# Optimization experiments

Hardware: AMD Instinct MI355X
Metric: run time of the kernel (lower is better)

## Reference

```python
import jax, jax.numpy as jnp
import numpy as np

B, T, F, U = 64, 256, 256, 1024  # batch, time, input feat, GRU units per layer


def setup_inputs() -> dict:
    key = jax.random.key(0)
    ks = jax.random.split(key, 16)
    rn = lambda k, shape, s: jax.random.normal(k, shape, dtype=jnp.float32) * s
    inp = {"inputs": rn(ks[0], (B, T, F), 1.0)}
    in_dims = [F, U, U]
    for i in range(3):
        inp[f"state{i}"] = rn(ks[1 + i], (B, U), 0.1)
        inp[f"W{i}"] = rn(ks[4 + 3 * i], (in_dims[i], 3 * U), 0.05)  # input kernel [in, 3u]
        inp[f"U{i}"] = rn(ks[5 + 3 * i], (U, 3 * U), 0.05)           # recurrent kernel [u, 3u]
        inp[f"b{i}"] = jnp.zeros((2, 3 * U), dtype=jnp.float32)       # [input_bias; recurrent_bias]
    return inp


def _gru_layer(x, h0, W, Ur, b):
    # Keras GRU, reset_after=True, recurrent_activation=sigmoid, activation=tanh.
    u = h0.shape[-1]
    gx = jnp.einsum('btf,fg->btg', x, W) + b[0]  # precompute input projections for all steps

    def step(h, gxt):
        rec = h @ Ur + b[1]                       # [B, 3u]
        z = jax.nn.sigmoid(gxt[:, :u] + rec[:, :u])
        r = jax.nn.sigmoid(gxt[:, u:2 * u] + rec[:, u:2 * u])
        hh = jnp.tanh(gxt[:, 2 * u:] + r * rec[:, 2 * u:])
        hn = z * h + (1.0 - z) * hh
        return hn, hn

    h_last, ys = jax.lax.scan(step, h0, jnp.swapaxes(gx, 0, 1))  # scan over time
    return jnp.swapaxes(ys, 0, 1), h_last


def reference(inputs, state0, state1, state2, W0, U0, b0, W1, U1, b1, W2, U2, b2):
    x, s0 = _gru_layer(inputs, state0, W0, U0, b0)
    x, s1 = _gru_layer(x, state1, W1, U1, b1)
    x, s2 = _gru_layer(x, state2, W2, U2, b2)
    return x, s0, s1, s2
```

## Files before the change

kernel.cpp:

```cpp
#include <hip/hip_runtime.h>
#include <hip/hip_fp16.h>


typedef _Float16 half8 __attribute__((ext_vector_type(8)));
typedef float f32x4 __attribute__((ext_vector_type(4)));

#define TSTEPS 256
#define UDIM 1024
#define G3U 3072
#define GRIDB 64

__device__ __forceinline__ f32x4 mfma16(half8 a, half8 b, f32x4 c) {
    return __builtin_amdgcn_mfma_f32_16x16x32_f16(a, b, c, 0, 0, 0);
}

__device__ __forceinline__ half8 load_h_agent(const _Float16* p) {
    union { unsigned long long u[2]; half8 h; } un;
    const unsigned long long* q = (const unsigned long long*)p;
    un.u[0] = __hip_atomic_load(q,     __ATOMIC_RELAXED, __HIP_MEMORY_SCOPE_AGENT);
    un.u[1] = __hip_atomic_load(q + 1, __ATOMIC_RELAXED, __HIP_MEMORY_SCOPE_AGENT);
    return un.h;
}

__global__ void f32_to_f16(const float* __restrict__ src, _Float16* __restrict__ dst, int n) {
    int i = blockIdx.x * blockDim.x + threadIdx.x;
    int st = gridDim.x * blockDim.x;
    for (; i < n; i += st) dst[i] = (_Float16)src[i];
}

__global__ void pack_weights(const float* __restrict__ W, const float* __restrict__ Ur,
                             _Float16* __restrict__ Bp, int KIN, int KC) {
    int idx = blockIdx.x * blockDim.x + threadIdx.x;
    int total = 192 * KC * 64;
    int st = gridDim.x * blockDim.x;
    for (; idx < total; idx += st) {
        int lane = idx & 63;
        int kc = (idx >> 6) % KC;
        int nt = idx / (KC * 64);
        int col = nt * 16 + (lane & 15);
        int k0 = kc * 32 + (lane >> 4) * 8;
        half8 v;
#pragma unroll
        for (int i = 0; i < 8; ++i) {
            int k = k0 + i;
            float f = (k < KIN) ? W[(size_t)k * G3U + col]
                                : Ur[(size_t)(k - KIN) * G3U + col];
            v[i] = (_Float16)f;
        }
        *(half8*)(Bp + (size_t)idx * 8) = v;
    }
}

struct LayerArgs {
    const _Float16* xcur;
    const _Float16* h0h;
    const float* state;
    const _Float16* Bp;
    const float* bias;
    _Float16* yown;
    float* fxout;
    float* sout;
    unsigned* own_cnt;
    const unsigned* prod_cnt;
};

using RedT = f32x4 (*)[4][2][64];

template <int KIN, bool XA>
__device__ __forceinline__ void gru_body(const LayerArgs& A, int blk, RedT red) {
    const int tid = threadIdx.x;
    const int lane = tid & 63;
    const int wid = tid >> 6;
    const int col = lane & 15;
    const int lrow = lane >> 4;
    const int klane0 = lrow * 8;
    const int j = blk * 16 + col;
    constexpr int KC = (KIN + UDIM) >> 5;
    constexpr int KCW = KC >> 3;
    constexpr int KINC = KIN >> 5;
    const int ck0 = wid * KCW, ck1 = ck0 + KCW;

    const float b0z = A.bias[j],           b1z = A.bias[G3U + j];
    const float b0r = A.bias[UDIM + j],    b1r = A.bias[G3U + UDIM + j];
    const float b0h = A.bias[2*UDIM + j],  b1h = A.bias[G3U + 2*UDIM + j];

    float hreg[4] = {0.f, 0.f, 0.f, 0.f};
    if (wid < 4) {
#pragma unroll
        for (int e = 0; e < 4; ++e) {
            int m = wid * 16 + lrow * 4 + e;
            hreg[e] = A.state[(size_t)m * UDIM + j];
        }
    }

    const _Float16* bpz = A.Bp + (size_t)(blk)       * KC * 512 + lane * 8;
    const _Float16* bpr = A.Bp + (size_t)(64 + blk)  * KC * 512 + lane * 8;
    const _Float16* bph = A.Bp + (size_t)(128 + blk) * KC * 512 + lane * 8;

    for (int t = 0; t < TSTEPS; ++t) {
        if (tid == 0) {
            if (t > 0) {
                unsigned tgt = (unsigned)(GRIDB * t);
                while (__hip_atomic_load(A.own_cnt, __ATOMIC_RELAXED,
                                         __HIP_MEMORY_SCOPE_AGENT) < tgt)
                    __builtin_amdgcn_s_sleep(2);
            }
            if (XA) {
                unsigned tgt2 = (unsigned)(GRIDB * (t + 1));
                while (__hip_atomic_load(A.prod_cnt, __ATOMIC_RELAXED,
                                         __HIP_MEMORY_SCOPE_AGENT) < tgt2)
                    __builtin_amdgcn_s_sleep(2);
            }
        }
        __syncthreads();

        f32x4 accz[4], accr[4], acchx[4], acchr[4];
#pragma unroll
        for (int m4 = 0; m4 < 4; ++m4) {
            accz[m4] = (f32x4){0.f,0.f,0.f,0.f};
            accr[m4] = (f32x4){0.f,0.f,0.f,0.f};
            acchx[m4] = (f32x4){0.f,0.f,0.f,0.f};
            acchr[m4] = (f32x4){0.f,0.f,0.f,0.f};
        }
        const _Float16* xr[4];
        const _Float16* hr[4];
#pragma unroll
        for (int m4 = 0; m4 < 4; ++m4) {
            int rm = m4 * 16 + (lane & 15);
            xr[m4] = A.xcur + ((size_t)rm * TSTEPS + t) * KIN + klane0;
            hr[m4] = (t == 0) ? (A.h0h + (size_t)rm * UDIM + klane0)
                              : (A.yown + ((size_t)rm * TSTEPS + (t - 1)) * UDIM + klane0);
        }
        int cxe = ck1 < KINC ? ck1 : KINC;
#pragma unroll 2
        for (int ck = ck0; ck < cxe; ++ck) {
            half8 bz = *(const half8*)(bpz + (size_t)ck * 512);
            half8 br = *(const half8*)(bpr + (size_t)ck * 512);
            half8 bh = *(const half8*)(bph + (size_t)ck * 512);
            int off = ck * 32;
#pragma unroll
            for (int m4 = 0; m4 < 4; ++m4) {
                half8 a = XA ? load_h_agent(xr[m4] + off)
                             : *(const half8*)(xr[m4] + off);
                accz[m4]  = mfma16(a, bz, accz[m4]);
                accr[m4]  = mfma16(a, br, accr[m4]);
                acchx[m4] = mfma16(a, bh, acchx[m4]);
            }
        }
        int chs = ck0 > KINC ? ck0 : KINC;
#pragma unroll 2
        for (int ck = chs; ck < ck1; ++ck) {
            half8 bz = *(const half8*)(bpz + (size_t)ck * 512);
            half8 br = *(const half8*)(bpr + (size_t)ck * 512);
            half8 bh = *(const half8*)(bph + (size_t)ck * 512);
            int off = (ck - KINC) * 32;
#pragma unroll
            for (int m4 = 0; m4 < 4; ++m4) {
                half8 a = load_h_agent(hr[m4] + off);
                accz[m4]  = mfma16(a, bz, accz[m4]);
                accr[m4]  = mfma16(a, br, accr[m4]);
                acchr[m4] = mfma16(a, bh, acchr[m4]);
            }
        }

        f32x4 fz = {0.f,0.f,0.f,0.f}, fr = {0.f,0.f,0.f,0.f};
        f32x4 fhx = {0.f,0.f,0.f,0.f}, fhr = {0.f,0.f,0.f,0.f};
        for (int p = 0; p < 2; ++p) {
#pragma unroll
            for (int m4 = 0; m4 < 4; ++m4) {
                red[wid][m4][0][lane] = p ? acchx[m4] : accz[m4];
                red[wid][m4][1][lane] = p ? acchr[m4] : accr[m4];
            }
            __syncthreads();
            if (wid < 4) {
                f32x4 s0 = {0.f,0.f,0.f,0.f}, s1 = {0.f,0.f,0.f,0.f};
#pragma unroll
                for (int s = 0; s < 8; ++s) {
                    s0 += red[s][wid][0][lane];
                    s1 += red[s][wid][1][lane];
                }
                if (p == 0) { fz = s0; fr = s1; } else { fhx = s0; fhr = s1; }
            }
            __syncthreads();
        }

        if (wid < 4) {
#pragma unroll
            for (int e = 0; e < 4; ++e) {
                float zp = fz[e] + b0z + b1z;
                float rp = fr[e] + b0r + b1r;
                float z = 1.f / (1.f + expf(-zp));
                float r = 1.f / (1.f + expf(-rp));
                float hh = tanhf(fhx[e] + b0h + r * (fhr[e] + b1h));
                float hn = z * hreg[e] + (1.f - z) * hh;
                hreg[e] = hn;
                int m = wid * 16 + lrow * 4 + e;
                size_t yi = ((size_t)m * TSTEPS + t) * UDIM + j;
                union { _Float16 f; unsigned short u; } cv;
                cv.f = (_Float16)hn;
                unsigned pu = (unsigned)(unsigned short)__shfl_xor((int)(unsigned)cv.u, 1, 64);
                if (!(col & 1)) {
                    unsigned val = ((unsigned)cv.u) | (pu << 16);
                    __hip_atomic_store((unsigned*)(A.yown + yi), val,
                                       __ATOMIC_RELAXED, __HIP_MEMORY_SCOPE_AGENT);
                }
                if (A.fxout) A.fxout[yi] = hn;
                if (t == TSTEPS - 1) A.sout[(size_t)m * UDIM + j] = hn;
            }
        }

        __syncthreads();
        if (tid == 0)
            __hip_atomic_fetch_add(A.own_cnt, 1u, __ATOMIC_RELAXED,
                                   __HIP_MEMORY_SCOPE_AGENT);
    }
}

__global__ __launch_bounds__(512, 1) void gru_fused(LayerArgs a0, LayerArgs a1, LayerArgs a2) {
    __shared__ f32x4 red[8][4][2][64];
    int lay = blockIdx.x >> 6;
    int blk = blockIdx.x & 63;
    if (lay == 0)      gru_body<256,  false>(a0, blk, red);
    else if (lay == 1) gru_body<1024, true >(a1, blk, red);
    else               gru_body<1024, true >(a2, blk, red);
}

extern "C" void kernel_launch(void* const* d_in, const int* in_sizes, int n_in,
                              void* d_out, int out_size, void* d_ws, size_t ws_size,
                              hipStream_t stream) {
    (void)in_sizes; (void)n_in; (void)out_size; (void)ws_size;

    char* ws = (char*)d_ws;
    size_t off = 0;
    auto take = [&](size_t bytes) -> char* {
        char* p = ws + off;
        off += (bytes + 255) & ~(size_t)255;
        return p;
    };
    unsigned* counters = (unsigned*)take(1024);
    _Float16* h0h0 = (_Float16*)take((size_t)65536 * 2);
    _Float16* h0h1 = (_Float16*)take((size_t)65536 * 2);
    _Float16* h0h2 = (_Float16*)take((size_t)65536 * 2);
    _Float16* xin  = (_Float16*)take((size_t)4194304 * 2);
    _Float16* y0   = (_Float16*)take((size_t)16777216 * 2);
    _Float16* y1   = (_Float16*)take((size_t)16777216 * 2);
    _Float16* y2   = (_Float16*)take((size_t)16777216 * 2);
    _Float16* Bp0  = (_Float16*)take((size_t)192 * 40 * 512 * 2);
    _Float16* Bp1  = (_Float16*)take((size_t)192 * 64 * 512 * 2);
    _Float16* Bp2  = (_Float16*)take((size_t)192 * 64 * 512 * 2);

    hipMemsetAsync(counters, 0, 1024, stream);

    f32_to_f16<<<2048, 256, 0, stream>>>((const float*)d_in[0], xin, 4194304);
    f32_to_f16<<<64, 256, 0, stream>>>((const float*)d_in[1], h0h0, 65536);
    f32_to_f16<<<64, 256, 0, stream>>>((const float*)d_in[5], h0h1, 65536);
    f32_to_f16<<<64, 256, 0, stream>>>((const float*)d_in[9], h0h2, 65536);

    pack_weights<<<1920, 256, 0, stream>>>((const float*)d_in[2], (const float*)d_in[3],
                                           Bp0, 256, 40);
    pack_weights<<<3072, 256, 0, stream>>>((const float*)d_in[6], (const float*)d_in[7],
                                           Bp1, 1024, 64);
    pack_weights<<<3072, 256, 0, stream>>>((const float*)d_in[10], (const float*)d_in[11],
                                           Bp2, 1024, 64);

    float* xout = (float*)d_out;
    float* souts = xout + (size_t)16777216;

    LayerArgs a0 = { xin, h0h0, (const float*)d_in[1], Bp0, (const float*)d_in[4],
                     y0, nullptr, souts + 0, counters + 0, nullptr };
    LayerArgs a1 = { y0, h0h1, (const float*)d_in[5], Bp1, (const float*)d_in[8],
                     y1, nullptr, souts + 65536, counters + 64, counters + 0 };
    LayerArgs a2 = { y1, h0h2, (const float*)d_in[9], Bp2, (const float*)d_in[12],
                     y2, xout, souts + 131072, counters + 128, counters + 64 };

    gru_fused<<<192, 512, 0, stream>>>(a0, a1, a2);
}
```

Before: 5.272 ms.

## Replace global counters with per-block flags and per-wave polling, single reduction pass

Each block now publishes its progress in its own padded flag slot instead of incrementing one shared atomic counter. Every wavefront polls all 64 producer flags itself, and only right before it needs the data. Input-half waves can therefore start on the previous layer's output while hidden-half waves wait on the recurrent state. The two-pass LDS reduction becomes one pass with a single barrier, and the activations use fast __expf formulas. This removes contended atomics and serialized waits from the per-step critical path, at the cost of more polling traffic and slightly reduced precision in the activations.

```diff
diff --git a/kernel.cpp b/kernel.cpp
--- a/kernel.cpp
+++ b/kernel.cpp
@@ -20,6 +20,16 @@
     un.u[0] = __hip_atomic_load(q,     __ATOMIC_RELAXED, __HIP_MEMORY_SCOPE_AGENT);
     un.u[1] = __hip_atomic_load(q + 1, __ATOMIC_RELAXED, __HIP_MEMORY_SCOPE_AGENT);
     return un.h;
+}
+
+__device__ __forceinline__ void poll_flags(const unsigned* f, unsigned tgt) {
+    const unsigned* p = f + (threadIdx.x & 63) * 32;
+    for (;;) {
+        unsigned v = __hip_atomic_load(p, __ATOMIC_RELAXED, __HIP_MEMORY_SCOPE_AGENT);
+        if (__all((int)(v >= tgt))) break;
+        __builtin_amdgcn_s_sleep(2);
+    }
+    asm volatile("" ::: "memory");
 }
 
 __global__ void f32_to_f16(const float* __restrict__ src, _Float16* __restrict__ dst, int n) {
@@ -60,14 +70,12 @@
     _Float16* yown;
     float* fxout;
     float* sout;
-    unsigned* own_cnt;
-    const unsigned* prod_cnt;
+    unsigned* own_flags;
+    const unsigned* prod_flags;
 };
 
-using RedT = f32x4 (*)[4][2][64];
-
 template <int KIN, bool XA>
-__device__ __forceinline__ void gru_body(const LayerArgs& A, int blk, RedT red) {
+__device__ __forceinline__ void gru_body(const LayerArgs& A, int blk, f32x4* red) {
     const int tid = threadIdx.x;
     const int lane = tid & 63;
     const int wid = tid >> 6;
@@ -78,11 +86,15 @@
     constexpr int KC = (KIN + UDIM) >> 5;
     constexpr int KCW = KC >> 3;
     constexpr int KINC = KIN >> 5;
+    constexpr int NS = (KIN == UDIM) ? 3 : 4;
+    constexpr int HS = (NS == 3) ? 2 : 3;
     const int ck0 = wid * KCW, ck1 = ck0 + KCW;
-
-    const float b0z = A.bias[j],           b1z = A.bias[G3U + j];
-    const float b0r = A.bias[UDIM + j],    b1r = A.bias[G3U + UDIM + j];
-    const float b0h = A.bias[2*UDIM + j],  b1h = A.bias[G3U + 2*UDIM + j];
+    const bool has_x = ck0 < KINC;
+    const bool has_h = ck1 > KINC;
+
+    const float bsz = A.bias[j] + A.bias[G3U + j];
+    const float bsr = A.bias[UDIM + j] + A.bias[G3U + UDIM + j];
+    const float b0h = A.bias[2*UDIM + j], b1h = A.bias[G3U + 2*UDIM + j];
 
     float hreg[4] = {0.f, 0.f, 0.f, 0.f};
     if (wid < 4) {
@@ -98,30 +110,13 @@
     const _Float16* bph = A.Bp + (size_t)(128 + blk) * KC * 512 + lane * 8;
 
     for (int t = 0; t < TSTEPS; ++t) {
-        if (tid == 0) {
-            if (t > 0) {
-                unsigned tgt = (unsigned)(GRIDB * t);
-                while (__hip_atomic_load(A.own_cnt, __ATOMIC_RELAXED,
-                                         __HIP_MEMORY_SCOPE_AGENT) < tgt)
-                    __builtin_amdgcn_s_sleep(2);
-            }
-            if (XA) {
-                unsigned tgt2 = (unsigned)(GRIDB * (t + 1));
-                while (__hip_atomic_load(A.prod_cnt, __ATOMIC_RELAXED,
-                                         __HIP_MEMORY_SCOPE_AGENT) < tgt2)
-                    __builtin_amdgcn_s_sleep(2);
-            }
-        }
-        __syncthreads();
-
-        f32x4 accz[4], accr[4], acchx[4], acchr[4];
-#pragma unroll
-        for (int m4 = 0; m4 < 4; ++m4) {
-            accz[m4] = (f32x4){0.f,0.f,0.f,0.f};
-            accr[m4] = (f32x4){0.f,0.f,0.f,0.f};
-            acchx[m4] = (f32x4){0.f,0.f,0.f,0.f};
-            acchr[m4] = (f32x4){0.f,0.f,0.f,0.f};
-        }
+        f32x4 acc[4][4];
+#pragma unroll
+        for (int s = 0; s < 4; ++s)
+#pragma unroll
+            for (int m4 = 0; m4 < 4; ++m4)
+                acc[s][m4] = (f32x4){0.f, 0.f, 0.f, 0.f};
+
         const _Float16* xr[4];
         const _Float16* hr[4];
 #pragma unroll
@@ -131,6 +126,8 @@
             hr[m4] = (t == 0) ? (A.h0h + (size_t)rm * UDIM + klane0)
                               : (A.yown + ((size_t)rm * TSTEPS + (t - 1)) * UDIM + klane0);
         }
+
+        if (XA && has_x) poll_flags(A.prod_flags, (unsigned)(t + 1));
         int cxe = ck1 < KINC ? ck1 : KINC;
 #pragma unroll 2
         for (int ck = ck0; ck < cxe; ++ck) {
@@ -142,11 +139,12 @@
             for (int m4 = 0; m4 < 4; ++m4) {
                 half8 a = XA ? load_h_agent(xr[m4] + off)
                              : *(const half8*)(xr[m4] + off);
-                accz[m4]  = mfma16(a, bz, accz[m4]);
-                accr[m4]  = mfma16(a, br, accr[m4]);
-                acchx[m4] = mfma16(a, bh, acchx[m4]);
-            }
-        }
+                acc[0][m4] = mfma16(a, bz, acc[0][m4]);
+                acc[1][m4] = mfma16(a, br, acc[1][m4]);
+                acc[2][m4] = mfma16(a, bh, acc[2][m4]);
+            }
+        }
+        if (has_h && t > 0) poll_flags(A.own_flags, (unsigned)t);
         int chs = ck0 > KINC ? ck0 : KINC;
 #pragma unroll 2
         for (int ck = chs; ck < ck1; ++ck) {
@@ -157,41 +155,42 @@
 #pragma unroll
             for (int m4 = 0; m4 < 4; ++m4) {
                 half8 a = load_h_agent(hr[m4] + off);
-                accz[m4]  = mfma16(a, bz, accz[m4]);
-                accr[m4]  = mfma16(a, br, accr[m4]);
-                acchr[m4] = mfma16(a, bh, acchr[m4]);
-            }
-        }
-
-        f32x4 fz = {0.f,0.f,0.f,0.f}, fr = {0.f,0.f,0.f,0.f};
-        f32x4 fhx = {0.f,0.f,0.f,0.f}, fhr = {0.f,0.f,0.f,0.f};
-        for (int p = 0; p < 2; ++p) {
-#pragma unroll
-            for (int m4 = 0; m4 < 4; ++m4) {
-                red[wid][m4][0][lane] = p ? acchx[m4] : accz[m4];
-                red[wid][m4][1][lane] = p ? acchr[m4] : accr[m4];
-            }
-            __syncthreads();
-            if (wid < 4) {
-                f32x4 s0 = {0.f,0.f,0.f,0.f}, s1 = {0.f,0.f,0.f,0.f};
-#pragma unroll
-                for (int s = 0; s < 8; ++s) {
-                    s0 += red[s][wid][0][lane];
-                    s1 += red[s][wid][1][lane];
+                acc[0][m4] = mfma16(a, bz, acc[0][m4]);
+                acc[1][m4] = mfma16(a, br, acc[1][m4]);
+                acc[HS][m4] = mfma16(a, bh, acc[HS][m4]);
+            }
+        }
+
+#pragma unroll
+        for (int m4 = 0; m4 < 4; ++m4)
+#pragma unroll
+            for (int s = 0; s < NS; ++s)
+                red[(size_t)(((wid * 4 + m4) * NS + s) * 64 + lane)] = acc[s][m4];
+        __syncthreads();
+
+        if (wid < 4) {
+            f32x4 fz = {0.f,0.f,0.f,0.f}, fr = {0.f,0.f,0.f,0.f};
+            f32x4 fhx = {0.f,0.f,0.f,0.f}, fhr = {0.f,0.f,0.f,0.f};
+#pragma unroll
+            for (int s = 0; s < 8; ++s) {
+                fz += red[(size_t)(((s * 4 + wid) * NS + 0) * 64 + lane)];
+                fr += red[(size_t)(((s * 4 + wid) * NS + 1) * 64 + lane)];
+                if (NS == 4) {
+                    fhx += red[(size_t)(((s * 4 + wid) * NS + 2) * 64 + lane)];
+                    fhr += red[(size_t)(((s * 4 + wid) * NS + 3) * 64 + lane)];
+                } else {
+                    f32x4 v = red[(size_t)(((s * 4 + wid) * NS + 2) * 64 + lane)];
+                    if (s < 4) fhx += v; else fhr += v;
                 }
-                if (p == 0) { fz = s0; fr = s1; } else { fhx = s0; fhr = s1; }
-            }
-            __syncthreads();
-        }
-
-        if (wid < 4) {
+            }
 #pragma unroll
             for (int e = 0; e < 4; ++e) {
-                float zp = fz[e] + b0z + b1z;
-                float rp = fr[e] + b0r + b1r;
-                float z = 1.f / (1.f + expf(-zp));
-                float r = 1.f / (1.f + expf(-rp));
-                float hh = tanhf(fhx[e] + b0h + r * (fhr[e] + b1h));
+                float zp = fz[e] + bsz;
+                float rp = fr[e] + bsr;
+                float z = 1.f / (1.f + __expf(-zp));
+                float r = 1.f / (1.f + __expf(-rp));
+                float ha = fhx[e] + b0h + r * (fhr[e] + b1h);
+                float hh = 2.f / (1.f + __expf(-2.f * ha)) - 1.f;
                 float hn = z * hreg[e] + (1.f - z) * hh;
                 hreg[e] = hn;
                 int m = wid * 16 + lrow * 4 + e;
@@ -211,13 +210,13 @@
 
         __syncthreads();
         if (tid == 0)
-            __hip_atomic_fetch_add(A.own_cnt, 1u, __ATOMIC_RELAXED,
-                                   __HIP_MEMORY_SCOPE_AGENT);
+            __hip_atomic_store(A.own_flags + blk * 32, (unsigned)(t + 1),
+                               __ATOMIC_RELAXED, __HIP_MEMORY_SCOPE_AGENT);
     }
 }
 
 __global__ __launch_bounds__(512, 1) void gru_fused(LayerArgs a0, LayerArgs a1, LayerArgs a2) {
-    __shared__ f32x4 red[8][4][2][64];
+    __shared__ f32x4 red[8192];
     int lay = blockIdx.x >> 6;
     int blk = blockIdx.x & 63;
     if (lay == 0)      gru_body<256,  false>(a0, blk, red);
@@ -237,7 +236,7 @@
         off += (bytes + 255) & ~(size_t)255;
         return p;
     };
-    unsigned* counters = (unsigned*)take(1024);
+    unsigned* flags = (unsigned*)take(32768);
     _Float16* h0h0 = (_Float16*)take((size_t)65536 * 2);
     _Float16* h0h1 = (_Float16*)take((size_t)65536 * 2);
     _Float16* h0h2 = (_Float16*)take((size_t)65536 * 2);
@@ -249,7 +248,7 @@
     _Float16* Bp1  = (_Float16*)take((size_t)192 * 64 * 512 * 2);
     _Float16* Bp2  = (_Float16*)take((size_t)192 * 64 * 512 * 2);
 
-    hipMemsetAsync(counters, 0, 1024, stream);
+    hipMemsetAsync(flags, 0, 32768, stream);
 
     f32_to_f16<<<2048, 256, 0, stream>>>((const float*)d_in[0], xin, 4194304);
     f32_to_f16<<<64, 256, 0, stream>>>((const float*)d_in[1], h0h0, 65536);
@@ -266,12 +265,16 @@
     float* xout = (float*)d_out;
     float* souts = xout + (size_t)16777216;
 
+    unsigned* flags0 = flags;
+    unsigned* flags1 = flags + 2048;
+    unsigned* flags2 = flags + 4096;
+
     LayerArgs a0 = { xin, h0h0, (const float*)d_in[1], Bp0, (const float*)d_in[4],
-                     y0, nullptr, souts + 0, counters + 0, nullptr };
+                     y0, nullptr, souts + 0, flags0, nullptr };
     LayerArgs a1 = { y0, h0h1, (const float*)d_in[5], Bp1, (const float*)d_in[8],
-                     y1, nullptr, souts + 65536, counters + 64, counters + 0 };
+                     y1, nullptr, souts + 65536, flags1, flags0 };
     LayerArgs a2 = { y1, h0h2, (const float*)d_in[9], Bp2, (const float*)d_in[12],
-                     y2, xout, souts + 131072, counters + 128, counters + 64 };
+                     y2, xout, souts + 131072, flags2, flags1 };
 
     gru_fused<<<192, 512, 0, stream>>>(a0, a1, a2);
 }
```

After: 4.747 ms. 10.0% less time.
